# Performance work log

Hardware: AMD Instinct MI355X
Metric: run time of the kernel (lower is better)

## Reference

```python
import jax, jax.numpy as jnp
import numpy as np

TAU = 0.1
LAMBD = 0.75
EPS = 1e-8  # torch cosine_similarity norm clamp


def setup_inputs() -> dict:
    key = jax.random.key(0)
    k1, k2 = jax.random.split(key)
    B, D = 8192, 768
    v = jax.random.normal(k1, (B, D), dtype=jnp.float32)
    u = jax.random.normal(k2, (B, D), dtype=jnp.float32)
    return {"v": v, "u": u}


def reference(v, u):
    # Batched equivalent of the per-sample Python loop:
    # cos(v_i, u_j) = <v_i/||v_i||, u_j/||u_j||>, with torch's eps clamp on norms.
    v = v.astype(jnp.float32)
    u = u.astype(jnp.float32)
    vn = v / jnp.maximum(jnp.linalg.norm(v, axis=1, keepdims=True), EPS)
    un = u / jnp.maximum(jnp.linalg.norm(u, axis=1, keepdims=True), EPS)
    sim = jnp.einsum('id,jd->ij', vn, un) / TAU  # [B, B] logits
    diag = jnp.diagonal(sim)
    # image->text: -log( exp(sim_ii) / sum_j exp(sim_ij) )
    loss_it = jax.nn.logsumexp(sim, axis=1) - diag
    # text->image: -log( exp(sim_ii) / sum_j exp(sim_ji) )
    loss_ti = jax.nn.logsumexp(sim, axis=0) - diag
    # In the torch source text_image calls .item(), detaching it from autograd.
    loss_ti = jax.lax.stop_gradient(loss_ti)
    return jnp.mean(LAMBD * loss_it + (1.0 - LAMBD) * loss_ti)
```

## Files before the change

kernel.cpp:

```cpp
#include <hip/hip_runtime.h>
#include <hip/hip_bf16.h>

typedef unsigned char u8;
typedef unsigned short u16;
typedef unsigned int u32;
typedef float f32x16 __attribute__((ext_vector_type(16)));
typedef int i32x4 __attribute__((ext_vector_type(4)));
typedef int i32x8 __attribute__((ext_vector_type(8)));

#define B_SZ 8192
#define D_SZ 768
#define TAU_INV 10.0f
#define ESCALE 0.014088818758681283f
#define FP4_SCALE 32.0f
#define SCHRAU_K1 118185.58f
#define SCHRAU_K2 1064879685.0f


__device__ __forceinline__ u32 fp4_enc(float x) {
    float y = fabsf(x);
    u32 n = (u32)(y >= 0.25f) + (u32)(y >= 0.75f) + (u32)(y >= 1.25f) +
            (u32)(y >= 1.75f) + (u32)(y >= 2.5f)  + (u32)(y >= 3.5f) +
            (u32)(y >= 5.0f);
    return n | (x < 0.f ? 8u : 0u);
}

__device__ __forceinline__ u16 fp4_pack4(float x, float y, float z, float w) {
    return (u16)(fp4_enc(x) | (fp4_enc(y) << 4) | (fp4_enc(z) << 8) | (fp4_enc(w) << 12));
}

__global__ __launch_bounds__(256) void norm_kernel(const float4* __restrict__ v,
                                                   const float4* __restrict__ u,
                                                   u16* __restrict__ vn,
                                                   u16* __restrict__ un,
                                                   float* __restrict__ diag) {
    const int wid = threadIdx.x >> 6, lane = threadIdx.x & 63;
    const int row = blockIdx.x * 4 + wid;
    const float4* vr = v + (size_t)row * 192;
    const float4* ur = u + (size_t)row * 192;
    float4 a[3], b[3];
    float sv = 0.f, su = 0.f, sd = 0.f;
#pragma unroll
    for (int c = 0; c < 3; ++c) {
        a[c] = vr[lane + 64 * c];
        b[c] = ur[lane + 64 * c];
        sv += a[c].x * a[c].x + a[c].y * a[c].y + a[c].z * a[c].z + a[c].w * a[c].w;
        su += b[c].x * b[c].x + b[c].y * b[c].y + b[c].z * b[c].z + b[c].w * b[c].w;
        sd += a[c].x * b[c].x + a[c].y * b[c].y + a[c].z * b[c].z + a[c].w * b[c].w;
    }
#pragma unroll
    for (int m = 1; m < 64; m <<= 1) {
        sv += __shfl_xor(sv, m);
        su += __shfl_xor(su, m);
        sd += __shfl_xor(sd, m);
    }
    const float iv = FP4_SCALE / fmaxf(sqrtf(sv), 1e-8f);
    const float iu = FP4_SCALE / fmaxf(sqrtf(su), 1e-8f);
    const int rg = row >> 5, rr = row & 31;
#pragma unroll
    for (int c = 0; c < 3; ++c) {
        u16 pa = fp4_pack4(a[c].x * iv, a[c].y * iv, a[c].z * iv, a[c].w * iv);
        u16 pb = fp4_pack4(b[c].x * iu, b[c].y * iu, b[c].z * iu, b[c].w * iu);
        const int e = lane + 64 * c;
        const int idx = (rg * 12 + (e >> 4)) * 512 + ((e >> 3) & 1) * 256 + rr * 8 + (e & 7);
        vn[idx] = pa;
        un[idx] = pb;
    }
    if (lane == 0) diag[row] = sd * iv * iu * TAU_INV / (FP4_SCALE * FP4_SCALE);
}

__device__ __forceinline__ i32x8 ldfrag4(const u8* __restrict__ base, u32 off) {
    i32x4 lo = *(const i32x4*)(base + off);
    return __builtin_shufflevector(lo, lo, 0, 1, 2, 3, 0, 1, 2, 3);
}

__device__ __forceinline__ f32x16 mx_mfma4(i32x8 a, i32x8 b, f32x16 c) {
    return __builtin_amdgcn_mfma_scale_f32_32x32x64_f8f6f4(
        a, b, c, 4, 4, 0, 0x7F7F7F7F, 0, 0x7F7F7F7F);
}

__global__ __launch_bounds__(256, 4) void simexp_kernel(const u8* __restrict__ vn,
                                                        const u8* __restrict__ un,
                                                        float* __restrict__ rowP,
                                                        float* __restrict__ colP) {
    __shared__ float rowLds[2][128];
    __shared__ float colLds[2][128];

    const int tid  = threadIdx.x;
    const int wid  = tid >> 6;
    const int lane = tid & 63;
    const int l32  = lane & 31;
    const int h    = lane >> 5;
    const int wr = wid >> 1, wc = wid & 1;

    const int id = blockIdx.x;
    const int chunk = id >> 6;
    const int li = id & 63;
    const int rb = ((chunk >> 3) << 3) + (li >> 3);
    const int cb = ((chunk & 7) << 3) + (li & 7);

    const int aBase = __builtin_amdgcn_readfirstlane((rb * 4 + wr * 2) * 12288);
    const int bBase = __builtin_amdgcn_readfirstlane((cb * 4 + wc * 2) * 12288);
    const u8* __restrict__ A0 = vn + aBase;
    const u8* __restrict__ A1 = A0 + 12288;
    const u8* __restrict__ B0 = un + bBase;
    const u8* __restrict__ B1 = B0 + 12288;
    u32 voff = (u32)lane * 16;

    f32x16 acc[2][2];
#pragma unroll
    for (int i = 0; i < 2; ++i)
#pragma unroll
        for (int j = 0; j < 2; ++j)
#pragma unroll
            for (int r = 0; r < 16; ++r) acc[i][j][r] = 0.f;

    i32x8 fa[2][2], fb[2][2];

#define LOAD_SLOT(s)                        \
    {                                       \
        fa[s][0] = ldfrag4(A0, voff);       \
        fa[s][1] = ldfrag4(A1, voff);       \
        fb[s][0] = ldfrag4(B0, voff);       \
        fb[s][1] = ldfrag4(B1, voff);       \
        voff += 1024;                       \
    }
#define MFMA_SLOT(s)                                          \
    {                                                         \
        acc[0][0] = mx_mfma4(fa[s][0], fb[s][0], acc[0][0]);  \
        acc[1][0] = mx_mfma4(fa[s][1], fb[s][0], acc[1][0]);  \
        acc[0][1] = mx_mfma4(fa[s][0], fb[s][1], acc[0][1]);  \
        acc[1][1] = mx_mfma4(fa[s][1], fb[s][1], acc[1][1]);  \
    }

    LOAD_SLOT(0)
#pragma unroll 1
    for (int it = 0; it < 12; it += 2) {
        LOAD_SLOT(1)
        MFMA_SLOT(0)
        if (it + 2 < 12) LOAD_SLOT(0)
        MFMA_SLOT(1)
    }

    float rowAcc[32];
    float colAcc[2];
#pragma unroll
    for (int t = 0; t < 32; ++t) rowAcc[t] = 0.f;
    colAcc[0] = 0.f; colAcc[1] = 0.f;
#pragma unroll
    for (int i = 0; i < 2; ++i)
#pragma unroll
        for (int j = 0; j < 2; ++j)
#pragma unroll
            for (int r = 0; r < 16; ++r) {
                float t = fmaf(acc[i][j][r], SCHRAU_K1, SCHRAU_K2);
                float e = __int_as_float((int)t);
                rowAcc[i * 16 + r] += e;
                colAcc[j] += e;
            }
#pragma unroll
    for (int m = 1; m < 32; m <<= 1)
#pragma unroll
        for (int t = 0; t < 32; ++t) rowAcc[t] += __shfl_xor(rowAcc[t], m);
    colAcc[0] += __shfl_xor(colAcc[0], 32);
    colAcc[1] += __shfl_xor(colAcc[1], 32);

#pragma unroll
    for (int i = 0; i < 2; ++i)
#pragma unroll
        for (int t = 0; t < 16; ++t)
            if (l32 == t) {
                int row = wr * 64 + i * 32 + (t & 3) + 8 * (t >> 2) + 4 * h;
                rowLds[wc][row] = rowAcc[i * 16 + t];
            }
    if (h == 0) {
#pragma unroll
        for (int j = 0; j < 2; ++j)
            colLds[wr][wc * 64 + j * 32 + l32] = colAcc[j];
    }
    __syncthreads();
    if (tid < 128) {
        rowP[(size_t)cb * B_SZ + rb * 128 + tid] = rowLds[0][tid] + rowLds[1][tid];
    } else {
        const int t = tid - 128;
        colP[(size_t)rb * B_SZ + cb * 128 + t] = colLds[0][t] + colLds[1][t];
    }
}

__global__ __launch_bounds__(256) void finalize_kernel(const float* __restrict__ rowP,
                                                       const float* __restrict__ colP,
                                                       const float* __restrict__ diag,
                                                       float* __restrict__ out) {
    const int i = blockIdx.x * 256 + threadIdx.x;
    float rs = 0.f, cs = 0.f;
#pragma unroll 8
    for (int p = 0; p < 64; ++p) {
        rs += rowP[(size_t)p * B_SZ + i];
        cs += colP[(size_t)p * B_SZ + i];
    }
    float contrib = (0.75f * logf(rs) + 0.25f * logf(cs) - diag[i]) * (1.0f / (float)B_SZ);
#pragma unroll
    for (int m = 1; m < 64; m <<= 1) contrib += __shfl_xor(contrib, m);
    __shared__ float red[4];
    const int wid = threadIdx.x >> 6, lane = threadIdx.x & 63;
    if (lane == 0) red[wid] = contrib;
    __syncthreads();
    if (threadIdx.x == 0) atomicAdd(out, red[0] + red[1] + red[2] + red[3]);
}

extern "C" void kernel_launch(void* const* d_in, const int* in_sizes, int n_in,
                              void* d_out, int out_size, void* d_ws, size_t ws_size,
                              hipStream_t stream) {
    const float* v = (const float*)d_in[0];
    const float* u = (const float*)d_in[1];
    char* ws = (char*)d_ws;
    u16* vn4   = (u16*)(ws);
    u16* un4   = (u16*)(ws + 3145728);
    float* dg  = (float*)(ws + 6291456);
    float* rwp = (float*)(ws + 6324224);
    float* clp = (float*)(ws + 8421376);
    float* out = (float*)d_out;

    hipMemsetAsync(out, 0, sizeof(float), stream);
    hipLaunchKernelGGL(norm_kernel, dim3(2048), dim3(256), 0, stream,
                       (const float4*)v, (const float4*)u, vn4, un4, dg);
    hipLaunchKernelGGL(simexp_kernel, dim3(4096), dim3(256), 0, stream,
                       (const u8*)vn4, (const u8*)un4, rwp, clp);
    hipLaunchKernelGGL(finalize_kernel, dim3(B_SZ / 256), dim3(256), 0, stream, rwp, clp, dg, out);
}
```

Before: 138.0 us.

## Use transpose-style butterfly reduction for row sums and pack epilogue math

The epilogue's row-sum reduction changes from 32 values each shuffled across 5 butterfly stages to a recursive-halving exchange, where each stage swaps half of the partial sums with the partner lane. This cuts the shuffle count sharply. The exp approximation and accumulation are rewritten on float2 vectors so the compiler can emit packed FP32 ops. MFMA issue is also wrapped in s_setprio, and the unused upper half of the fp4 fragment is left undefined instead of duplicated. The per-lane select logic adds some ALU work and is easy to get wrong in the final row index mapping.

```diff
diff --git a/kernel.cpp b/kernel.cpp
--- a/kernel.cpp
+++ b/kernel.cpp
@@ -5,6 +5,7 @@
 typedef unsigned short u16;
 typedef unsigned int u32;
 typedef float f32x16 __attribute__((ext_vector_type(16)));
+typedef float f32x2 __attribute__((ext_vector_type(2)));
 typedef int i32x4 __attribute__((ext_vector_type(4)));
 typedef int i32x8 __attribute__((ext_vector_type(8)));
 
@@ -71,7 +72,7 @@
 
 __device__ __forceinline__ i32x8 ldfrag4(const u8* __restrict__ base, u32 off) {
     i32x4 lo = *(const i32x4*)(base + off);
-    return __builtin_shufflevector(lo, lo, 0, 1, 2, 3, 0, 1, 2, 3);
+    return __builtin_shufflevector(lo, lo, 0, 1, 2, 3, -1, -1, -1, -1);
 }
 
 __device__ __forceinline__ f32x16 mx_mfma4(i32x8 a, i32x8 b, f32x16 c) {
@@ -127,10 +128,12 @@
     }
 #define MFMA_SLOT(s)                                          \
     {                                                         \
+        __builtin_amdgcn_s_setprio(1);                        \
         acc[0][0] = mx_mfma4(fa[s][0], fb[s][0], acc[0][0]);  \
         acc[1][0] = mx_mfma4(fa[s][1], fb[s][0], acc[1][0]);  \
         acc[0][1] = mx_mfma4(fa[s][0], fb[s][1], acc[0][1]);  \
         acc[1][1] = mx_mfma4(fa[s][1], fb[s][1], acc[1][1]);  \
+        __builtin_amdgcn_s_setprio(0);                        \
     }
 
     LOAD_SLOT(0)
@@ -142,41 +145,67 @@
         MFMA_SLOT(1)
     }
 
-    float rowAcc[32];
-    float colAcc[2];
-#pragma unroll
-    for (int t = 0; t < 32; ++t) rowAcc[t] = 0.f;
-    colAcc[0] = 0.f; colAcc[1] = 0.f;
+    f32x2 val2[16];
+    f32x2 cacc2[2];
+#pragma unroll
+    for (int p = 0; p < 16; ++p) { val2[p].x = 0.f; val2[p].y = 0.f; }
+    cacc2[0].x = 0.f; cacc2[0].y = 0.f;
+    cacc2[1].x = 0.f; cacc2[1].y = 0.f;
 #pragma unroll
     for (int i = 0; i < 2; ++i)
 #pragma unroll
         for (int j = 0; j < 2; ++j)
 #pragma unroll
-            for (int r = 0; r < 16; ++r) {
-                float t = fmaf(acc[i][j][r], SCHRAU_K1, SCHRAU_K2);
-                float e = __int_as_float((int)t);
-                rowAcc[i * 16 + r] += e;
-                colAcc[j] += e;
+            for (int r = 0; r < 16; r += 2) {
+                f32x2 a;
+                a.x = acc[i][j][r];
+                a.y = acc[i][j][r + 1];
+                f32x2 t = a * SCHRAU_K1 + SCHRAU_K2;
+                f32x2 e;
+                e.x = __int_as_float((int)t.x);
+                e.y = __int_as_float((int)t.y);
+                val2[i * 8 + (r >> 1)] += e;
+                cacc2[j] += e;
             }
-#pragma unroll
-    for (int m = 1; m < 32; m <<= 1)
-#pragma unroll
-        for (int t = 0; t < 32; ++t) rowAcc[t] += __shfl_xor(rowAcc[t], m);
-    colAcc[0] += __shfl_xor(colAcc[0], 32);
-    colAcc[1] += __shfl_xor(colAcc[1], 32);
-
-#pragma unroll
-    for (int i = 0; i < 2; ++i)
-#pragma unroll
-        for (int t = 0; t < 16; ++t)
-            if (l32 == t) {
-                int row = wr * 64 + i * 32 + (t & 3) + 8 * (t >> 2) + 4 * h;
-                rowLds[wc][row] = rowAcc[i * 16 + t];
-            }
-    if (h == 0) {
-#pragma unroll
-        for (int j = 0; j < 2; ++j)
-            colLds[wr][wc * 64 + j * 32 + l32] = colAcc[j];
+
+#pragma unroll
+    for (int m = 16; m >= 2; m >>= 1) {
+        const int n = m >> 1;
+        const bool hi = (l32 & m) != 0;
+#pragma unroll
+        for (int p = 0; p < n; ++p) {
+            f32x2 a = val2[p], b = val2[p + n];
+            f32x2 x, y;
+            x.x = hi ? b.x : a.x;  x.y = hi ? b.y : a.y;
+            y.x = hi ? a.x : b.x;  y.y = hi ? a.y : b.y;
+            f32x2 s;
+            s.x = __shfl_xor(y.x, m);
+            s.y = __shfl_xor(y.y, m);
+            val2[p] = x + s;
+        }
+    }
+    {
+        f32x2 s;
+        s.x = __shfl_xor(val2[0].x, 1);
+        s.y = __shfl_xor(val2[0].y, 1);
+        val2[0] += s;
+    }
+    {
+        const int q = (l32 >> 1) & 15;
+        const int t = 2 * q + (l32 & 1);
+        const int i = t >> 4, r = t & 15;
+        const int row = wr * 64 + i * 32 + (r & 3) + 8 * (r >> 2) + 4 * h;
+        rowLds[wc][row] = (l32 & 1) ? val2[0].y : val2[0].x;
+    }
+    {
+        float c0 = cacc2[0].x + cacc2[0].y;
+        float c1 = cacc2[1].x + cacc2[1].y;
+        c0 += __shfl_xor(c0, 32);
+        c1 += __shfl_xor(c1, 32);
+        if (h == 0) {
+            colLds[wr][wc * 64 + l32]      = c0;
+            colLds[wr][wc * 64 + 32 + l32] = c1;
+        }
     }
     __syncthreads();
     if (tid < 128) {
```

Result: faster. 131.3 us (-4.8%).
